# Kernel optimization log

Measured on AMD Instinct MI355X. Metric: run time of the kernel, lower is better.

## Reference

```python
import jax, jax.numpy as jnp
import numpy as np

EPS = 1e-12  # tf.math.l2_normalize epsilon

def _l2norm(a, axis):
    # tf.math.l2_normalize: a * rsqrt(max(sum(a^2), eps))
    sq = jnp.sum(a * a, axis=axis, keepdims=True)
    return a * jax.lax.rsqrt(jnp.maximum(sq, EPS))

def setup_inputs() -> dict:
    key = jax.random.key(0)
    k1, k2 = jax.random.split(key)
    B, D, N = 4096, 512, 5994
    x = jax.random.normal(k1, (B, D), dtype=jnp.float32)
    W = jax.random.normal(k2, (D, N), dtype=jnp.float32)
    return {"x": x, "W": W}

def reference(x, W):
    # Normalize x along feature dim (axis=-1 of x), W along axis=-1 (output_dim),
    # exactly as in the TF layer; the broadcast multiply + reduce over input_dim
    # is mathematically a matmul: out[b,n] = sum_d xn[b,d] * Wn[d,n].
    xn = _l2norm(x, axis=-1)          # (B, D)
    Wn = _l2norm(W, axis=-1)          # (D, N), normalized per input-dim row
    return jnp.einsum('bd,dn->bn', xn, Wn)  # (B, N)
```

## Files before the change

kernel.cpp:

```cpp
#include <hip/hip_runtime.h>
#include <hip/hip_bf16.h>

typedef __attribute__((ext_vector_type(8))) short short8;
typedef __attribute__((ext_vector_type(4))) float floatx4;

#define L2EPS 1e-12f

__device__ __forceinline__ unsigned short f2bf(float f) {
  union { float f; unsigned u; } c; c.f = f;
  unsigned u = c.u;
  unsigned r = (u + 0x7fffu + ((u >> 16) & 1u)) >> 16;
  return (unsigned short)r;
}

__device__ __forceinline__ void gload_lds16(const void* g, void* l) {
  __builtin_amdgcn_global_load_lds(
      (const __attribute__((address_space(1))) unsigned int*)g,
      (__attribute__((address_space(3))) unsigned int*)l,
      16, 0, 0);
}

__global__ __launch_bounds__(256) void wnorm_kernel(const float* __restrict__ W,
                                                    float* __restrict__ rnw, int N) {
  const int d = blockIdx.x;
  const float2* row2 = (const float2*)(W + (size_t)d * N);
  const int n2 = N >> 1;
  float s = 0.f;
  for (int i = threadIdx.x; i < n2; i += 256) {
    const float2 v = row2[i];
    s += v.x * v.x + v.y * v.y;
  }
  if (threadIdx.x == 0 && (N & 1)) {
    const float v = W[(size_t)d * N + (N - 1)];
    s += v * v;
  }
#pragma unroll
  for (int off = 32; off > 0; off >>= 1) s += __shfl_xor(s, off);
  __shared__ float red[4];
  if ((threadIdx.x & 63) == 0) red[threadIdx.x >> 6] = s;
  __syncthreads();
  if (threadIdx.x == 0) {
    const float t = red[0] + red[1] + red[2] + red[3];
    rnw[d] = rsqrtf(fmaxf(t, L2EPS));
  }
}

__global__ __launch_bounds__(256) void prep_kernel(const float* __restrict__ x,
                                                   const float* __restrict__ W,
                                                   const float* __restrict__ rnw,
                                                   unsigned short* __restrict__ xb,
                                                   unsigned short* __restrict__ BT,
                                                   int N, int nxb, int nwx) {
  const int bid = blockIdx.x;
  if (bid < nxb) {
    const int lane = threadIdx.x & 63;
    const int wave = threadIdx.x >> 6;
    const int row  = bid * 4 + wave;
    const float4* xr = (const float4*)(x + (size_t)row * 512);
    const float4 v0 = xr[lane * 2];
    const float4 v1 = xr[lane * 2 + 1];
    float s = v0.x*v0.x + v0.y*v0.y + v0.z*v0.z + v0.w*v0.w
            + v1.x*v1.x + v1.y*v1.y + v1.z*v1.z + v1.w*v1.w;
#pragma unroll
    for (int off = 32; off > 0; off >>= 1) s += __shfl_xor(s, off);
    const float r = rsqrtf(fmaxf(s, L2EPS));
    const float4 w0 = ((const float4*)rnw)[lane * 2];
    const float4 w1 = ((const float4*)rnw)[lane * 2 + 1];
    short8 o;
    o[0] = (short)f2bf(v0.x * r * w0.x); o[1] = (short)f2bf(v0.y * r * w0.y);
    o[2] = (short)f2bf(v0.z * r * w0.z); o[3] = (short)f2bf(v0.w * r * w0.w);
    o[4] = (short)f2bf(v1.x * r * w1.x); o[5] = (short)f2bf(v1.y * r * w1.y);
    o[6] = (short)f2bf(v1.z * r * w1.z); o[7] = (short)f2bf(v1.w * r * w1.w);
    *(short8*)(xb + (size_t)row * 512 + lane * 8) = o;
  } else {
    __shared__ unsigned short tile[32][33];
    const int wb = bid - nxb;
    const int n0 = (wb % nwx) * 32;
    const int d0 = (wb / nwx) * 32;
    const int tx = threadIdx.x & 31;
    const int ty = threadIdx.x >> 5;
#pragma unroll
    for (int i = 0; i < 4; ++i) {
      const int dl = ty + i * 8;
      const int n = n0 + tx;
      float v = 0.f;
      if (n < N) v = W[(size_t)(d0 + dl) * N + n];
      tile[tx][dl] = f2bf(v);
    }
    __syncthreads();
#pragma unroll
    for (int i = 0; i < 4; ++i) {
      const int nl = ty + i * 8;
      BT[(size_t)(n0 + nl) * 512 + d0 + tx] = tile[nl][tx];
    }
  }
}

#define NT 16

__global__ __launch_bounds__(512, 2) void gemm_kernel(
    const unsigned short* __restrict__ A,
    const unsigned short* __restrict__ BT,
    float* __restrict__ C,
    int N, int nbx, int nby) {
  __shared__ unsigned short As[4][256 * 32];
  __shared__ unsigned short Bs[4][256 * 32];

  const int tid = threadIdx.x;
  const int l   = tid & 63;
  const int w   = tid >> 6;
  const int wr  = w >> 2;
  const int wc  = w & 3;

  const int grid = nbx * nby;
  const int bid  = blockIdx.x;
  int swz = bid;
  if ((grid & 7) == 0) swz = (bid & 7) * (grid >> 3) + (bid >> 3);
  const int bx = swz / nby;
  const int by = swz % nby;
  const int row0 = by * 256;
  const int col0 = bx * 256;

  floatx4 acc[8][4];
#pragma unroll
  for (int m = 0; m < 8; ++m)
#pragma unroll
    for (int n = 0; n < 4; ++n)
      acc[m][n] = (floatx4){0.f, 0.f, 0.f, 0.f};

  const int srow = tid >> 2;
  const int sch  = ((tid & 3) ^ ((tid >> 3) & 3)) * 8;
  const unsigned short* Ag = A  + (size_t)(row0 + srow) * 512 + sch;
  const unsigned short* Bg = BT + (size_t)(col0 + srow) * 512 + sch;
  const int ldst = srow * 32 + (tid & 3) * 8;

#define STAGE(t_) do { \
    gload_lds16(Ag + (t_) * 32,                     &As[(t_) & 3][ldst]); \
    gload_lds16(Ag + (size_t)128 * 512 + (t_) * 32, &As[(t_) & 3][ldst + 4096]); \
    gload_lds16(Bg + (t_) * 32,                     &Bs[(t_) & 3][ldst]); \
    gload_lds16(Bg + (size_t)128 * 512 + (t_) * 32, &Bs[(t_) & 3][ldst + 4096]); \
  } while (0)
#define CFENCE asm volatile("" ::: "memory")

  const int ln15 = l & 15;
  const int qs   = (((l >> 4) ^ ((ln15 >> 1) & 3))) * 8;
  const int ab   = (wr * 128 + ln15) * 32 + qs;
  const int bb   = (wc * 64 + ln15) * 32 + qs;

  STAGE(0); STAGE(1); STAGE(2);
  asm volatile("s_waitcnt vmcnt(8)" ::: "memory");
  __builtin_amdgcn_s_barrier();
  CFENCE;

#pragma unroll
  for (int t = 0; t < NT; ++t) {
    const int b = t & 3;
    if (t + 3 < NT) STAGE(t + 3);
    CFENCE;
    short8 af[8], bf[4];
#pragma unroll
    for (int n = 0; n < 4; ++n) bf[n] = *(const short8*)&Bs[b][bb + n * 512];
#pragma unroll
    for (int m = 0; m < 8; ++m) af[m] = *(const short8*)&As[b][ab + m * 512];
    CFENCE;
    __builtin_amdgcn_s_setprio(1);
#pragma unroll
    for (int m = 0; m < 8; ++m)
#pragma unroll
      for (int n = 0; n < 4; ++n)
        acc[m][n] = __builtin_amdgcn_mfma_f32_16x16x32_bf16(af[m], bf[n], acc[m][n], 0, 0, 0);
    __builtin_amdgcn_s_setprio(0);
    CFENCE;
    if (t < NT - 3)       asm volatile("s_waitcnt vmcnt(8)" ::: "memory");
    else if (t == NT - 3) asm volatile("s_waitcnt vmcnt(4)" ::: "memory");
    else if (t == NT - 2) asm volatile("s_waitcnt vmcnt(0)" ::: "memory");
    if (t < NT - 1) {
      __builtin_amdgcn_s_barrier();
      CFENCE;
    }
  }

  const int rb = row0 + wr * 128 + (l >> 4) * 4;
  const int cb = col0 + wc * 64 + ln15;
#pragma unroll
  for (int m = 0; m < 8; ++m) {
#pragma unroll
    for (int r = 0; r < 4; ++r) {
      const size_t o = (size_t)(rb + m * 16 + r) * N + cb;
#pragma unroll
      for (int n = 0; n < 4; ++n) {
        if (cb + n * 16 < N) C[o + n * 16] = acc[m][n][r];
      }
    }
  }
#undef STAGE
#undef CFENCE
}

extern "C" void kernel_launch(void* const* d_in, const int* in_sizes, int n_in,
                              void* d_out, int out_size, void* d_ws, size_t ws_size,
                              hipStream_t stream) {
  const float* x = (const float*)d_in[0];
  const float* W = (const float*)d_in[1];
  float* out = (float*)d_out;

  const int D = 512;
  const int B = in_sizes[0] / D;
  const int N = in_sizes[1] / D;
  const int Npad = ((N + 255) / 256) * 256;

  char* ws = (char*)d_ws;
  unsigned short* xb  = (unsigned short*)ws;
  unsigned short* BTb = (unsigned short*)(ws + (size_t)B * D * 2);
  float* rnw = (float*)(ws + (size_t)B * D * 2 + (size_t)Npad * D * 2);

  const int nby = B / 256;
  const int nbx = Npad / 256;
  const int nxb = B / 4;
  const int nwx = Npad / 32;
  const int nwb = nwx * (D / 32);

  wnorm_kernel<<<D, 256, 0, stream>>>(W, rnw, N);
  prep_kernel<<<nxb + nwb, 256, 0, stream>>>(x, W, rnw, xb, BTb, N, nxb, nwx);
  gemm_kernel<<<nbx * nby, 512, 0, stream>>>(xb, BTb, out, N, nbx, nby);
}
```

Baseline: 64.02 us.

## Restructure GEMM main loop to double-buffered K=64 tiles with interleaved staging

Replaces the 4-stage K=32 LDS ring with a 2-buffer K=64 layout and a new XOR swizzle. Global-to-LDS loads for the A and B halves are spread across four sub-phases per tile, each followed by a barrier, so memory traffic interleaves with MFMA work. This roughly halves the number of tile iterations but adds more barriers per tile, and the hand-placed vmcnt counts must stay exactly right for correctness.

```diff
diff --git a/kernel.cpp b/kernel.cpp
--- a/kernel.cpp
+++ b/kernel.cpp
@@ -96,15 +96,13 @@
   }
 }
 
-#define NT 16
-
 __global__ __launch_bounds__(512, 2) void gemm_kernel(
     const unsigned short* __restrict__ A,
     const unsigned short* __restrict__ BT,
     float* __restrict__ C,
     int N, int nbx, int nby) {
-  __shared__ unsigned short As[4][256 * 32];
-  __shared__ unsigned short Bs[4][256 * 32];
+  __shared__ unsigned short As[2][256 * 64];
+  __shared__ unsigned short Bs[2][256 * 64];
 
   const int tid = threadIdx.x;
   const int l   = tid & 63;
@@ -128,55 +126,90 @@
     for (int n = 0; n < 4; ++n)
       acc[m][n] = (floatx4){0.f, 0.f, 0.f, 0.f};
 
-  const int srow = tid >> 2;
-  const int sch  = ((tid & 3) ^ ((tid >> 3) & 3)) * 8;
-  const unsigned short* Ag = A  + (size_t)(row0 + srow) * 512 + sch;
-  const unsigned short* Bg = BT + (size_t)(col0 + srow) * 512 + sch;
-  const int ldst = srow * 32 + (tid & 3) * 8;
-
-#define STAGE(t_) do { \
-    gload_lds16(Ag + (t_) * 32,                     &As[(t_) & 3][ldst]); \
-    gload_lds16(Ag + (size_t)128 * 512 + (t_) * 32, &As[(t_) & 3][ldst + 4096]); \
-    gload_lds16(Bg + (t_) * 32,                     &Bs[(t_) & 3][ldst]); \
-    gload_lds16(Bg + (size_t)128 * 512 + (t_) * 32, &Bs[(t_) & 3][ldst + 4096]); \
+  const int srow = tid >> 3;
+  const int sch  = ((tid & 7) ^ (srow & 7)) * 8;
+  const unsigned short* Ap = A  + (size_t)(row0 + srow) * 512 + sch;
+  const unsigned short* Bp = BT + (size_t)(col0 + srow) * 512 + sch;
+  const int lo = tid * 8;
+
+#define STG_A(s_, h_, kt_) do { \
+    gload_lds16(Ap + (size_t)((h_) * 128) * 512 + (kt_) * 64,      &As[s_][((h_) * 128) * 64 + lo]); \
+    gload_lds16(Ap + (size_t)((h_) * 128 + 64) * 512 + (kt_) * 64, &As[s_][((h_) * 128 + 64) * 64 + lo]); \
+  } while (0)
+#define STG_B(s_, h_, kt_) do { \
+    gload_lds16(Bp + (size_t)((h_) * 128) * 512 + (kt_) * 64,      &Bs[s_][((h_) * 128) * 64 + lo]); \
+    gload_lds16(Bp + (size_t)((h_) * 128 + 64) * 512 + (kt_) * 64, &Bs[s_][((h_) * 128 + 64) * 64 + lo]); \
   } while (0)
 #define CFENCE asm volatile("" ::: "memory")
 
   const int ln15 = l & 15;
-  const int qs   = (((l >> 4) ^ ((ln15 >> 1) & 3))) * 8;
-  const int ab   = (wr * 128 + ln15) * 32 + qs;
-  const int bb   = (wc * 64 + ln15) * 32 + qs;
-
-  STAGE(0); STAGE(1); STAGE(2);
-  asm volatile("s_waitcnt vmcnt(8)" ::: "memory");
+  const int q4   = l >> 4;
+  const int e7   = ln15 & 7;
+  const int cs0  = ((q4) ^ e7) * 8;
+  const int cs1  = ((4 + q4) ^ e7) * 8;
+  const int abase = (wr * 128 + ln15) * 64;
+  const int bbase = (wc * 64 + ln15) * 64;
+
+  STG_A(0, 0, 0); STG_A(0, 1, 0);
+  STG_B(0, 0, 0); STG_B(0, 1, 0);
+  STG_B(1, 0, 1); STG_B(1, 1, 1);
+  asm volatile("s_waitcnt vmcnt(4)" ::: "memory");
   __builtin_amdgcn_s_barrier();
   CFENCE;
 
 #pragma unroll
-  for (int t = 0; t < NT; ++t) {
-    const int b = t & 3;
-    if (t + 3 < NT) STAGE(t + 3);
-    CFENCE;
-    short8 af[8], bf[4];
-#pragma unroll
-    for (int n = 0; n < 4; ++n) bf[n] = *(const short8*)&Bs[b][bb + n * 512];
-#pragma unroll
-    for (int m = 0; m < 8; ++m) af[m] = *(const short8*)&As[b][ab + m * 512];
-    CFENCE;
-    __builtin_amdgcn_s_setprio(1);
-#pragma unroll
-    for (int m = 0; m < 8; ++m)
-#pragma unroll
-      for (int n = 0; n < 4; ++n)
-        acc[m][n] = __builtin_amdgcn_mfma_f32_16x16x32_bf16(af[m], bf[n], acc[m][n], 0, 0, 0);
-    __builtin_amdgcn_s_setprio(0);
-    CFENCE;
-    if (t < NT - 3)       asm volatile("s_waitcnt vmcnt(8)" ::: "memory");
-    else if (t == NT - 3) asm volatile("s_waitcnt vmcnt(4)" ::: "memory");
-    else if (t == NT - 2) asm volatile("s_waitcnt vmcnt(0)" ::: "memory");
-    if (t < NT - 1) {
-      __builtin_amdgcn_s_barrier();
-      CFENCE;
+  for (int it = 0; it < 4; ++it) {
+#pragma unroll
+    for (int tt = 0; tt < 2; ++tt) {
+      short8 bf[4][2];
+      short8 af[2][2];
+#pragma unroll
+      for (int mp = 0; mp < 4; ++mp) {
+        if (mp == 0) {
+#pragma unroll
+          for (int n = 0; n < 4; ++n) {
+            bf[n][0] = *(const short8*)&Bs[tt][bbase + n * 1024 + cs0];
+            bf[n][1] = *(const short8*)&Bs[tt][bbase + n * 1024 + cs1];
+          }
+        }
+        af[0][0] = *(const short8*)&As[tt][abase + (2 * mp) * 1024 + cs0];
+        af[0][1] = *(const short8*)&As[tt][abase + (2 * mp) * 1024 + cs1];
+        af[1][0] = *(const short8*)&As[tt][abase + (2 * mp + 1) * 1024 + cs0];
+        af[1][1] = *(const short8*)&As[tt][abase + (2 * mp + 1) * 1024 + cs1];
+        if (tt == 0) {
+          if (mp == 1)           STG_A(1, 0, 2 * it + 1);
+          if (mp == 2) {         STG_A(1, 1, 2 * it + 1);
+            if (it < 3)          STG_B(0, 0, 2 * it + 2); }
+          if (mp == 3 && it < 3) STG_B(0, 1, 2 * it + 2);
+        } else {
+          if (mp == 1 && it < 3) STG_A(0, 0, 2 * it + 2);
+          if (mp == 2 && it < 3) STG_A(0, 1, 2 * it + 2);
+          if (mp == 3 && it < 3) { STG_B(1, 0, 2 * it + 3); STG_B(1, 1, 2 * it + 3); }
+        }
+        CFENCE;
+        if (mp == 3 && tt == 0) {
+          if (it < 3) asm volatile("s_waitcnt vmcnt(4)" ::: "memory");
+          else        asm volatile("s_waitcnt vmcnt(0)" ::: "memory");
+        }
+        if (mp == 3 && tt == 1 && it < 3)
+          asm volatile("s_waitcnt vmcnt(4)" ::: "memory");
+        if (!(it == 3 && tt == 1)) {
+          __builtin_amdgcn_s_barrier();
+          CFENCE;
+        }
+        __builtin_amdgcn_s_setprio(1);
+#pragma unroll
+        for (int j = 0; j < 2; ++j)
+#pragma unroll
+          for (int n = 0; n < 4; ++n) {
+            acc[2 * mp + j][n] = __builtin_amdgcn_mfma_f32_16x16x32_bf16(
+                af[j][0], bf[n][0], acc[2 * mp + j][n], 0, 0, 0);
+            acc[2 * mp + j][n] = __builtin_amdgcn_mfma_f32_16x16x32_bf16(
+                af[j][1], bf[n][1], acc[2 * mp + j][n], 0, 0, 0);
+          }
+        __builtin_amdgcn_s_setprio(0);
+        CFENCE;
+      }
     }
   }
 
@@ -193,7 +226,8 @@
       }
     }
   }
-#undef STAGE
+#undef STG_A
+#undef STG_B
 #undef CFENCE
 }
 
```

After: 61.38 us. 4.1% less time.
